# Optimization experiments

Hardware: AMD Instinct MI355X
Metric: run time of the kernel (lower is better)

Reference implementation:

```python
import jax, jax.numpy as jnp
import numpy as np

S, R, HC = 38, 340, 128      # num_s, num_r, h_channels
SC, RC, NO = 4, 3, 7          # s_channels, r_channels, num_o
L = 4                         # num_layers
B = 512                       # graphs per batch
N = B * (S + R)               # total nodes = 193536
E = 3_072_000                 # total edges
EPS = 1e-5


def leaky(x):
    return jnp.where(x > 0, x, 0.2 * x)


def batchnorm(x, w, b):
    # BatchNorm1d in training mode: batch stats, biased variance
    m = jnp.mean(x, axis=0)
    v = jnp.var(x, axis=0)
    return (x - m) * jax.lax.rsqrt(v + EPS) * w + b


def setup_inputs() -> dict:
    key = jax.random.key(0)
    ks = jax.random.split(key, 16)
    f32 = jnp.float32

    def w(k, shape, fan_in):
        return jax.random.normal(k, shape, f32) * (1.0 / np.sqrt(fan_in))

    return {
        "s_x": jax.random.normal(ks[0], (B * S, SC), f32),
        "r_x": jax.random.normal(ks[1], (B * R, RC + 5), f32),
        "edge_index": jax.random.randint(ks[2], (2, E), 0, N, dtype=jnp.int32),
        "bn_s_w": jnp.ones((SC,), f32),
        "bn_s_b": jnp.zeros((SC,), f32),
        "bn_r_w": jnp.ones((RC,), f32),
        "bn_r_b": jnp.zeros((RC,), f32),
        "lin_s_w": w(ks[3], (SC, HC), SC),
        "lin_r_w": w(ks[4], (RC, HC), RC),
        "conv_w": w(ks[5], (L, HC, HC), HC),
        "conv_b": jnp.zeros((L, HC), f32),
        "linr_w": w(ks[6], (S + R, NO), S + R),
        "linr_b": jnp.zeros((NO,), f32),
        "lino_w1": w(ks[7], (5, HC), 5),
        "lino_b1": jnp.zeros((HC,), f32),
        "lino_w2": w(ks[8], (HC, NO), HC),
        "lino_b2": jnp.zeros((NO,), f32),
    }


def reference(s_x, r_x, edge_index, bn_s_w, bn_s_b, bn_r_w, bn_r_b,
              lin_s_w, lin_r_w, conv_w, conv_b, linr_w, linr_b,
              lino_w1, lino_b1, lino_w2, lino_b2):
    Bn = r_x.shape[0] // R
    r_full = r_x.reshape(Bn, R, RC + 5)
    o_x = r_full[:, 0, RC:]                       # [B, 5]
    r = r_full[:, :, :RC].reshape(-1, RC)         # [B*R, 3]

    s = leaky(batchnorm(s_x, bn_s_w, bn_s_b) @ lin_s_w)   # [B*S, HC]
    r = leaky(batchnorm(r, bn_r_w, bn_r_b) @ lin_r_w)     # [B*R, HC]

    x = jnp.concatenate([s.reshape(Bn, S, HC), r.reshape(Bn, R, HC)], axis=1)
    x = x.reshape(-1, HC)                          # [N, HC]
    n = x.shape[0]

    # GCN normalization with self loops (computed once, shared by all layers)
    loops = jnp.arange(n, dtype=edge_index.dtype)
    src = jnp.concatenate([edge_index[0], loops])
    dst = jnp.concatenate([edge_index[1], loops])
    deg = jax.ops.segment_sum(jnp.ones_like(src, jnp.float32), dst, num_segments=n)
    dinv = jax.lax.rsqrt(deg)                      # deg >= 1 via self loops
    norm = (dinv[src] * dinv[dst])[:, None]        # [E+N, 1]

    for l in range(L):
        xw = x @ conv_w[l]                         # transform
        agg = jax.ops.segment_sum(norm * xw[src], dst, num_segments=n)
        x = x + leaky(agg + conv_b[l])             # residual + LeakyReLU

    pooled = x.reshape(Bn, S + R, HC).mean(axis=-1)  # adaptive_avg_pool1d over channels -> [B, 378]
    z = jnp.exp(pooled @ linr_w + linr_b)
    z = z / (jnp.sum(z, axis=1, keepdims=True) + 1.0)

    o = leaky(o_x @ lino_w1 + lino_b1) @ lino_w2 + lino_b2
    return z * jnp.exp(o)
```

## Files before the change

kernel.cpp:

```cpp
#include <hip/hip_runtime.h>
#include <hip/hip_bf16.h>

#define SDIM 38
#define RDIM 340
#define HC   128
#define SC   4
#define RC   3
#define NO   7
#define LCONV 4
#define BATCH 512
#define SR   378
#define NN   (BATCH*SR)
#define NS   (BATCH*SDIM)
#define NR   (BATCH*RDIM)
#define EE   3072000
#define EPSV 1e-5f
#define NBUK 756
#define BCAP 4800
#define BK_BLOCKS 256
#define BK_EDGES  12000
#define NSB 76

typedef short v8s __attribute__((ext_vector_type(8)));
typedef float v4f __attribute__((ext_vector_type(4)));
typedef float v2f __attribute__((ext_vector_type(2)));

__device__ __forceinline__ float leaky(float v){ return v > 0.f ? v : 0.2f*v; }

__device__ __forceinline__ unsigned short f2bf(float f){
    union { float f; unsigned u; } v; v.f = f;
    unsigned r = v.u + 0x7fffu + ((v.u >> 16) & 1u);
    return (unsigned short)(r >> 16);
}
__device__ __forceinline__ float4 bf4_to_f4(uint2 p){
    float4 r;
    r.x = __uint_as_float(p.x << 16);
    r.y = __uint_as_float(p.x & 0xffff0000u);
    r.z = __uint_as_float(p.y << 16);
    r.w = __uint_as_float(p.y & 0xffff0000u);
    return r;
}
__device__ __forceinline__ float4 fp8x4_to_f4(unsigned u){
    v2f lo = __builtin_amdgcn_cvt_pk_f32_fp8((int)u, false);
    v2f hi = __builtin_amdgcn_cvt_pk_f32_fp8((int)u, true);
    return make_float4(lo.x, lo.y, hi.x, hi.y);
}
__device__ __forceinline__ unsigned f4_to_fp8x4(float a, float b, float c, float d){
    int v = 0;
    v = __builtin_amdgcn_cvt_pk_fp8_f32(a, b, v, false);
    v = __builtin_amdgcn_cvt_pk_fp8_f32(c, d, v, true);
    return (unsigned)v;
}

__global__ void stats_kernel(const float* __restrict__ s_x, const float* __restrict__ r_x,
                             float* __restrict__ stats){
    int tid = threadIdx.x;
    __shared__ float sh[256][8];
    if (blockIdx.x < NSB){
        int r = blockIdx.x*256 + tid;
        float4 v = make_float4(0.f,0.f,0.f,0.f);
        if (r < NS) v = *(const float4*)(s_x + (size_t)r*SC);
        sh[tid][0]=v.x; sh[tid][1]=v.y; sh[tid][2]=v.z; sh[tid][3]=v.w;
        sh[tid][4]=v.x*v.x; sh[tid][5]=v.y*v.y; sh[tid][6]=v.z*v.z; sh[tid][7]=v.w*v.w;
        __syncthreads();
        for (int s=128; s>0; s>>=1){
            if (tid < s){
                #pragma unroll
                for (int k=0;k<8;k++) sh[tid][k]+=sh[tid+s][k];
            }
            __syncthreads();
        }
        if (tid < 8) atomicAdd(&stats[tid], sh[0][tid]);
    } else {
        int r = (blockIdx.x - NSB)*256 + tid;
        float4 v = make_float4(0.f,0.f,0.f,0.f);
        if (r < NR) v = *(const float4*)(r_x + (size_t)r*8);
        sh[tid][0]=v.x; sh[tid][1]=v.y; sh[tid][2]=v.z;
        sh[tid][3]=v.x*v.x; sh[tid][4]=v.y*v.y; sh[tid][5]=v.z*v.z;
        sh[tid][6]=0.f; sh[tid][7]=0.f;
        __syncthreads();
        for (int s=128; s>0; s>>=1){
            if (tid < s){
                #pragma unroll
                for (int k=0;k<6;k++) sh[tid][k]+=sh[tid+s][k];
            }
            __syncthreads();
        }
        if (tid < 6) atomicAdd(&stats[8+tid], sh[0][tid]);
    }
}

__global__ void finalize_stats_kernel(float* __restrict__ st,
        const float* __restrict__ bn_s_w, const float* __restrict__ bn_s_b,
        const float* __restrict__ bn_r_w, const float* __restrict__ bn_r_b){
    int t = threadIdx.x;
    if (t < SC){
        float m  = st[t] * (1.f/NS);
        float var= st[4+t] * (1.f/NS) - m*m;
        float sc = rsqrtf(var + EPSV) * bn_s_w[t];
        st[16+t] = sc; st[20+t] = bn_s_b[t] - m*sc;
    } else if (t >= 8 && t < 8+RC){
        int k = t-8;
        float m  = st[8+k] * (1.f/NR);
        float var= st[11+k] * (1.f/NR) - m*m;
        float sc = rsqrtf(var + EPSV) * bn_r_w[k];
        st[24+k] = sc; st[27+k] = bn_r_b[k] - m*sc;
    }
}

__global__ void feature_kernel(const float* __restrict__ s_x, const float* __restrict__ r_x,
        const float* __restrict__ stats, const float* __restrict__ lin_s_w,
        const float* __restrict__ lin_r_w, unsigned short* __restrict__ xb){
    int node = blockIdx.x*4 + (threadIdx.x >> 6);
    int c0 = (threadIdx.x & 63) * 2;
    int b = node / SR;
    int p = node - b*SR;
    float a0, a1;
    if (p < SDIM){
        int row = b*SDIM + p;
        float4 v = *(const float4*)(s_x + (size_t)row*SC);
        float i0 = v.x*stats[16]+stats[20];
        float i1 = v.y*stats[17]+stats[21];
        float i2 = v.z*stats[18]+stats[22];
        float i3 = v.w*stats[19]+stats[23];
        a0 = i0*lin_s_w[c0] + i1*lin_s_w[HC+c0] + i2*lin_s_w[2*HC+c0] + i3*lin_s_w[3*HC+c0];
        a1 = i0*lin_s_w[c0+1] + i1*lin_s_w[HC+c0+1] + i2*lin_s_w[2*HC+c0+1] + i3*lin_s_w[3*HC+c0+1];
    } else {
        int row = b*RDIM + (p - SDIM);
        float4 v = *(const float4*)(r_x + (size_t)row*8);
        float i0 = v.x*stats[24]+stats[27];
        float i1 = v.y*stats[25]+stats[28];
        float i2 = v.z*stats[26]+stats[29];
        a0 = i0*lin_r_w[c0] + i1*lin_r_w[HC+c0] + i2*lin_r_w[2*HC+c0];
        a1 = i0*lin_r_w[c0+1] + i1*lin_r_w[HC+c0+1] + i2*lin_r_w[2*HC+c0+1];
    }
    a0 = leaky(a0); a1 = leaky(a1);
    unsigned pk = (unsigned)f2bf(a0) | ((unsigned)f2bf(a1) << 16);
    *(unsigned*)(xb + (size_t)node*HC + c0) = pk;
}

__global__ __launch_bounds__(256) void bucket_kernel(const int* __restrict__ src,
        const int* __restrict__ dst, int* __restrict__ bcnt,
        unsigned* __restrict__ bedge){
    __shared__ int hist[NBUK];
    __shared__ int cur[NBUK];
    int tid = threadIdx.x;
    int e0 = blockIdx.x * BK_EDGES;
    for (int b = tid; b < NBUK; b += 256) hist[b] = 0;
    __syncthreads();
    for (int j = tid; j < BK_EDGES; j += 256){
        int d = dst[e0 + j];
        atomicAdd(&hist[d >> 8], 1);
    }
    __syncthreads();
    for (int b = tid; b < NBUK; b += 256){
        int c = hist[b];
        cur[b] = (c > 0) ? atomicAdd(&bcnt[b], c) : 0;
    }
    __syncthreads();
    for (int j = tid; j < BK_EDGES; j += 256){
        int d = dst[e0 + j];
        int s = src[e0 + j];
        int b = d >> 8;
        int pos = atomicAdd(&cur[b], 1);
        bedge[(size_t)b*BCAP + pos] = ((unsigned)s << 8) | (unsigned)(d & 255);
    }
}

__global__ __launch_bounds__(256) void hist_kernel(const int* __restrict__ bcnt,
        int* __restrict__ bbase, const unsigned* __restrict__ bedge,
        int* __restrict__ rp, float* __restrict__ dinv){
    __shared__ int h[256];
    __shared__ int sc[256];
    __shared__ int pre[256];
    int b = blockIdx.x, tid = threadIdx.x;
    int ps = 0;
    for (int i = tid; i < NBUK; i += 256)
        if (i < b) ps += bcnt[i];
    pre[tid] = ps;
    h[tid] = 0;
    __syncthreads();
    for (int s=128; s>0; s>>=1){
        if (tid < s) pre[tid] += pre[tid+s];
        __syncthreads();
    }
    int base = pre[0];
    int n = bcnt[b];
    const unsigned* be = bedge + (size_t)b*BCAP;
    for (int j = tid; j < n; j += 256)
        atomicAdd(&h[be[j] & 255u], 1);
    __syncthreads();
    int v = h[tid];
    sc[tid] = v;
    __syncthreads();
    for (int off=1; off<256; off<<=1){
        int t = (tid >= off) ? sc[tid-off] : 0;
        __syncthreads();
        sc[tid] += t;
        __syncthreads();
    }
    int node = b*256 + tid;
    rp[node] = base + sc[tid] - v;
    dinv[node] = rsqrtf((float)(v + 1));
    if (tid == 0) bbase[b] = base;
    if (b == NBUK-1 && tid == 0) rp[NN] = EE;
}

__global__ __launch_bounds__(256) void build_kernel(const int* __restrict__ bcnt,
        const int* __restrict__ bbase, const unsigned* __restrict__ bedge,
        const int* __restrict__ rp, const float* __restrict__ dinv,
        int2* __restrict__ csr){
    __shared__ int cur[256];
    __shared__ float dlocal[256];
    __shared__ int2 stage[BCAP];
    int b = blockIdx.x, tid = threadIdx.x;
    int base = bbase[b];
    cur[tid] = rp[b*256 + tid] - base;
    dlocal[tid] = dinv[b*256 + tid];
    __syncthreads();
    int n = bcnt[b];
    const unsigned* be = bedge + (size_t)b*BCAP;
    for (int j = tid; j < n; j += 256){
        unsigned e = be[j];
        int dl = (int)(e & 255u);
        int s  = (int)(e >> 8);
        float w = dinv[s] * dlocal[dl];
        int pos = atomicAdd(&cur[dl], 1);
        stage[pos] = make_int2((int)((e & ~255u) >> 1), __float_as_int(w));
    }
    __syncthreads();
    int2* seg = csr + base;
    for (int j = tid; j < n; j += 256)
        seg[j] = stage[j];
}

__global__ void wswz_kernel(const float* __restrict__ conv_w, uint4* __restrict__ wswz){
    int l = blockIdx.x;
    const float* Wg = conv_w + (size_t)l*HC*HC;
    int tid = threadIdx.x;
    #pragma unroll
    for (int i=0;i<8;i++){
        int slot = tid + i*256;
        int g = slot >> 6;
        int ln = slot & 63;
        int nt = g >> 2, ks = g & 3;
        int q = ln >> 4, n = nt*16 + (ln & 15);
        int k0 = ks*32 + q*8;
        unsigned short h[8];
        #pragma unroll
        for (int j=0;j<8;j++) h[j] = f2bf(Wg[(size_t)(k0+j)*HC + n]);
        uint4 o;
        o.x = (unsigned)h[0] | ((unsigned)h[1]<<16);
        o.y = (unsigned)h[2] | ((unsigned)h[3]<<16);
        o.z = (unsigned)h[4] | ((unsigned)h[5]<<16);
        o.w = (unsigned)h[6] | ((unsigned)h[7]<<16);
        wswz[(size_t)l*2048 + slot] = o;
    }
}

__global__ __launch_bounds__(256) void gemm_kernel(const unsigned short* __restrict__ xb,
        const uint4* __restrict__ wswz, unsigned char* __restrict__ xw){
    __shared__ uint4 Wlds[2048];
    __shared__ unsigned short outb[64*136];
    int tid = threadIdx.x;
    #pragma unroll
    for (int i=0;i<8;i++){
        int slot = tid + i*256;
        Wlds[slot] = wswz[slot];
    }
    int lane = tid & 63, w = tid >> 6;
    int q = lane >> 4, m = lane & 15;
    int rowbase = blockIdx.x*128;
    v4f acc[2][8];
    #pragma unroll
    for (int rg=0;rg<2;rg++)
        #pragma unroll
        for (int nt=0;nt<8;nt++) acc[rg][nt] = (v4f){0.f,0.f,0.f,0.f};
    __syncthreads();
    #pragma unroll
    for (int rg=0; rg<2; rg++){
        int row = rowbase + rg*64 + w*16 + m;
        const v8s* arow = (const v8s*)(xb + (size_t)row*HC + q*8);
        #pragma unroll
        for (int ks=0; ks<4; ks++){
            v8s a = arow[ks*4];
            #pragma unroll
            for (int nt=0;nt<8;nt++){
                v8s b = *(const v8s*)&Wlds[(nt*4+ks)*64 + lane];
                acc[rg][nt] = __builtin_amdgcn_mfma_f32_16x16x32_bf16(a, b, acc[rg][nt], 0, 0, 0);
            }
        }
    }
    #pragma unroll
    for (int rg=0; rg<2; rg++){
        #pragma unroll
        for (int nt=0;nt<8;nt++){
            #pragma unroll
            for (int i=0;i<4;i++){
                outb[(w*16 + q*4 + i)*136 + nt*16 + m] = f2bf(acc[rg][nt][i]);
            }
        }
        __syncthreads();
        size_t gbase = (size_t)(rowbase + rg*64) * HC;
        #pragma unroll
        for (int i=0;i<4;i++){
            int c = tid + i*256;
            int r = c >> 4, j = c & 15;
            uint4 v = *(const uint4*)&outb[r*136 + j*8];
            float4 lo = bf4_to_f4(make_uint2(v.x, v.y));
            float4 hi = bf4_to_f4(make_uint2(v.z, v.w));
            uint2 o;
            o.x = f4_to_fp8x4(lo.x, lo.y, lo.z, lo.w);
            o.y = f4_to_fp8x4(hi.x, hi.y, hi.z, hi.w);
            *(uint2*)&xw[gbase + (size_t)r*HC + j*8] = o;
        }
        __syncthreads();
    }
}

__global__ __launch_bounds__(256) void agg_kernel(const unsigned char* __restrict__ xw,
        const int* __restrict__ rp, const int2* __restrict__ csr,
        const float* __restrict__ dinv, const float* __restrict__ bias,
        unsigned short* __restrict__ xb, float* __restrict__ pooled){
    int lane = threadIdx.x & 63;
    int node = blockIdx.x*4 + (threadIdx.x >> 6);
    int g  = lane >> 4;
    unsigned c8 = (lane & 15) * 8;
    int beg = rp[node], end = rp[node+1];

    float4 aL0 = make_float4(0.f,0.f,0.f,0.f), aH0 = aL0;
    float4 aL1 = aL0, aH1 = aL0;

    int j = beg + g;
    while (j + 4 < end){
        int2 e0 = csr[j];
        int2 e1 = csr[j+4];
        uint2 p0 = *(const uint2*)(xw + ((unsigned)e0.x + c8));
        uint2 p1 = *(const uint2*)(xw + ((unsigned)e1.x + c8));
        float w0 = __int_as_float(e0.y);
        float w1 = __int_as_float(e1.y);
        float4 lo0 = fp8x4_to_f4(p0.x);
        float4 hi0 = fp8x4_to_f4(p0.y);
        float4 lo1 = fp8x4_to_f4(p1.x);
        float4 hi1 = fp8x4_to_f4(p1.y);
        aL0.x += w0*lo0.x; aL0.y += w0*lo0.y; aL0.z += w0*lo0.z; aL0.w += w0*lo0.w;
        aH0.x += w0*hi0.x; aH0.y += w0*hi0.y; aH0.z += w0*hi0.z; aH0.w += w0*hi0.w;
        aL1.x += w1*lo1.x; aL1.y += w1*lo1.y; aL1.z += w1*lo1.z; aL1.w += w1*lo1.w;
        aH1.x += w1*hi1.x; aH1.y += w1*hi1.y; aH1.z += w1*hi1.z; aH1.w += w1*hi1.w;
        j += 8;
    }
    while (j < end){
        int2 e = csr[j];
        uint2 p = *(const uint2*)(xw + ((unsigned)e.x + c8));
        float w = __int_as_float(e.y);
        float4 lo = fp8x4_to_f4(p.x);
        float4 hi = fp8x4_to_f4(p.y);
        aL0.x += w*lo.x; aL0.y += w*lo.y; aL0.z += w*lo.z; aL0.w += w*lo.w;
        aH0.x += w*hi.x; aH0.y += w*hi.y; aH0.z += w*hi.z; aH0.w += w*hi.w;
        j += 4;
    }
    aL0.x += aL1.x; aL0.y += aL1.y; aL0.z += aL1.z; aL0.w += aL1.w;
    aH0.x += aH1.x; aH0.y += aH1.y; aH0.z += aH1.z; aH0.w += aH1.w;
    if (g == 0){
        float dn = dinv[node];
        float sw = dn*dn;
        uint2 p = *(const uint2*)(xw + ((unsigned)node*HC + c8));
        float4 lo = fp8x4_to_f4(p.x);
        float4 hi = fp8x4_to_f4(p.y);
        aL0.x += sw*lo.x; aL0.y += sw*lo.y; aL0.z += sw*lo.z; aL0.w += sw*lo.w;
        aH0.x += sw*hi.x; aH0.y += sw*hi.y; aH0.z += sw*hi.z; aH0.w += sw*hi.w;
    }
    #pragma unroll
    for (int m2 = 16; m2 <= 32; m2 <<= 1){
        aL0.x += __shfl_xor(aL0.x, m2, 64);
        aL0.y += __shfl_xor(aL0.y, m2, 64);
        aL0.z += __shfl_xor(aL0.z, m2, 64);
        aL0.w += __shfl_xor(aL0.w, m2, 64);
        aH0.x += __shfl_xor(aH0.x, m2, 64);
        aH0.y += __shfl_xor(aH0.y, m2, 64);
        aH0.z += __shfl_xor(aH0.z, m2, 64);
        aH0.w += __shfl_xor(aH0.w, m2, 64);
    }
    if (g == 0){
        float4 bL = *(const float4*)(bias + c8);
        float4 bH = *(const float4*)(bias + c8 + 4);
        size_t idx = (size_t)node*HC + c8;
        uint4 xp = *(const uint4*)(xb + idx);
        float4 xL = bf4_to_f4(make_uint2(xp.x, xp.y));
        float4 xH = bf4_to_f4(make_uint2(xp.z, xp.w));
        xL.x += leaky(aL0.x + bL.x);
        xL.y += leaky(aL0.y + bL.y);
        xL.z += leaky(aL0.z + bL.z);
        xL.w += leaky(aL0.w + bL.w);
        xH.x += leaky(aH0.x + bH.x);
        xH.y += leaky(aH0.y + bH.y);
        xH.z += leaky(aH0.z + bH.z);
        xH.w += leaky(aH0.w + bH.w);
        if (pooled == nullptr){
            uint4 pk;
            pk.x = (unsigned)f2bf(xL.x) | ((unsigned)f2bf(xL.y) << 16);
            pk.y = (unsigned)f2bf(xL.z) | ((unsigned)f2bf(xL.w) << 16);
            pk.z = (unsigned)f2bf(xH.x) | ((unsigned)f2bf(xH.y) << 16);
            pk.w = (unsigned)f2bf(xH.z) | ((unsigned)f2bf(xH.w) << 16);
            *(uint4*)(xb + idx) = pk;
        } else {
            float s = xL.x + xL.y + xL.z + xL.w + xH.x + xH.y + xH.z + xH.w;
            #pragma unroll
            for (int m2 = 1; m2 < 16; m2 <<= 1)
                s += __shfl_xor(s, m2, 64);
            if (lane == 0) pooled[node] = s * (1.f/128.f);
        }
    }
}

__global__ void head_kernel(const float* __restrict__ pooled, const float* __restrict__ r_x,
        const float* __restrict__ linr_w, const float* __restrict__ linr_b,
        const float* __restrict__ lino_w1, const float* __restrict__ lino_b1,
        const float* __restrict__ lino_w2, const float* __restrict__ lino_b2,
        float* __restrict__ out){
    int b = blockIdx.x, tid = threadIdx.x;
    __shared__ float red[128][8];
    __shared__ float hsh[128];
    __shared__ float zsh[8];
    float part[NO];
    #pragma unroll
    for (int j=0;j<NO;j++) part[j]=0.f;
    for (int i = tid; i < SR; i += 128){
        float pv = pooled[(size_t)b*SR + i];
        #pragma unroll
        for (int j=0;j<NO;j++) part[j] += pv * linr_w[i*NO + j];
    }
    #pragma unroll
    for (int j=0;j<NO;j++) red[tid][j] = part[j];
    const float* ox = r_x + (size_t)b*RDIM*8 + RC;
    float hv = lino_b1[tid];
    #pragma unroll
    for (int k=0;k<5;k++) hv += ox[k]*lino_w1[k*HC + tid];
    hsh[tid] = leaky(hv);
    __syncthreads();
    for (int s=64; s>0; s>>=1){
        if (tid < s){
            #pragma unroll
            for (int j=0;j<NO;j++) red[tid][j] += red[tid+s][j];
        }
        __syncthreads();
    }
    if (tid < NO) zsh[tid] = expf(red[0][tid] + linr_b[tid]);
    __syncthreads();
    if (tid < NO){
        float zsum = 0.f;
        #pragma unroll
        for (int j=0;j<NO;j++) zsum += zsh[j];
        float z = zsh[tid] / (zsum + 1.f);
        float o = lino_b2[tid];
        for (int cc=0; cc<HC; cc++) o += hsh[cc]*lino_w2[cc*NO + tid];
        out[b*NO + tid] = z * expf(o);
    }
}

extern "C" void kernel_launch(void* const* d_in, const int* in_sizes, int n_in,
                              void* d_out, int out_size, void* d_ws, size_t ws_size,
                              hipStream_t stream) {
    const float* s_x     = (const float*)d_in[0];
    const float* r_x     = (const float*)d_in[1];
    const int*   ei      = (const int*)d_in[2];
    const float* bn_s_w  = (const float*)d_in[3];
    const float* bn_s_b  = (const float*)d_in[4];
    const float* bn_r_w  = (const float*)d_in[5];
    const float* bn_r_b  = (const float*)d_in[6];
    const float* lin_s_w = (const float*)d_in[7];
    const float* lin_r_w = (const float*)d_in[8];
    const float* conv_w  = (const float*)d_in[9];
    const float* conv_b  = (const float*)d_in[10];
    const float* linr_w  = (const float*)d_in[11];
    const float* linr_b  = (const float*)d_in[12];
    const float* lino_w1 = (const float*)d_in[13];
    const float* lino_b1 = (const float*)d_in[14];
    const float* lino_w2 = (const float*)d_in[15];
    const float* lino_b2 = (const float*)d_in[16];
    float* out = (float*)d_out;

    char* ws = (char*)d_ws;
    size_t off = 0;
    auto alloc = [&](size_t bytes)->void*{
        void* p = ws + off;
        off = (off + bytes + 255) & ~(size_t)255;
        return p;
    };
    unsigned short* xb = (unsigned short*)alloc((size_t)NN*HC*2);
    unsigned char*  xw = (unsigned char*) alloc((size_t)NN*HC);
    float* dinv     = (float*)alloc((size_t)NN*4);
    int*   rp       = (int*)  alloc((size_t)(NN+1)*4);
    int2*  csr      = (int2*) alloc((size_t)EE*8);
    unsigned* bedge = (unsigned*)alloc((size_t)NBUK*BCAP*4);
    int*   bcnt     = (int*)  alloc((size_t)NBUK*4);
    int*   bbase    = (int*)  alloc((size_t)NBUK*4);
    float* stats    = (float*)alloc(64*4);
    float* pooled   = (float*)alloc((size_t)NN*4);
    uint4* wswz     = (uint4*)alloc((size_t)LCONV*2048*16);

    hipMemsetAsync(bcnt, 0, (size_t)NBUK*4, stream);
    hipMemsetAsync(stats, 0, 64*4, stream);

    stats_kernel<<<NSB + (NR+255)/256, 256, 0, stream>>>(s_x, r_x, stats);
    finalize_stats_kernel<<<1, 64, 0, stream>>>(stats, bn_s_w, bn_s_b, bn_r_w, bn_r_b);
    feature_kernel<<<NN/4, 256, 0, stream>>>(s_x, r_x, stats, lin_s_w, lin_r_w, xb);
    wswz_kernel<<<LCONV, 256, 0, stream>>>(conv_w, wswz);

    bucket_kernel<<<BK_BLOCKS, 256, 0, stream>>>(ei, ei + EE, bcnt, bedge);
    hist_kernel<<<NBUK, 256, 0, stream>>>(bcnt, bbase, bedge, rp, dinv);
    build_kernel<<<NBUK, 256, 0, stream>>>(bcnt, bbase, bedge, rp, dinv, csr);

    for (int l = 0; l < LCONV; l++){
        gemm_kernel<<<NN/128, 256, 0, stream>>>(xb, wswz + (size_t)l*2048, xw);
        agg_kernel<<<NN/4, 256, 0, stream>>>(xw, rp, csr, dinv, conv_b + (size_t)l*HC,
                                             xb, (l == LCONV-1) ? pooled : nullptr);
    }

    head_kernel<<<BATCH, 128, 0, stream>>>(pooled, r_x, linr_w, linr_b,
                                           lino_w1, lino_b1, lino_w2, lino_b2, out);
}
```

Measured before the change: 744.6 us.

## Store node features in MFMA-panel layout and use packed fp8 conversion in aggregation

The bf16 node feature buffer moves from row-major to a 16-row panel layout that matches the MFMA A-operand fragment order. The GEMM can then read each lane's fragment as one contiguous coalesced 16-byte load per panel instead of strided row loads. The feature and aggregation kernels are changed to write and read this layout, and the feature kernel now produces 8 channels per thread. The aggregation accumulators are also rewritten as packed float2 multiply-adds on the pk fp8 conversions. The risk is that the residual read-modify-write in aggregation now does scattered 16-byte accesses into panels.

```diff
diff --git a/kernel.cpp b/kernel.cpp
--- a/kernel.cpp
+++ b/kernel.cpp
@@ -21,6 +21,7 @@
 #define BK_EDGES  12000
 #define NSB 76
 
+
 typedef short v8s __attribute__((ext_vector_type(8)));
 typedef float v4f __attribute__((ext_vector_type(4)));
 typedef float v2f __attribute__((ext_vector_type(2)));
@@ -39,11 +40,6 @@
     r.z = __uint_as_float(p.y << 16);
     r.w = __uint_as_float(p.y & 0xffff0000u);
     return r;
-}
-__device__ __forceinline__ float4 fp8x4_to_f4(unsigned u){
-    v2f lo = __builtin_amdgcn_cvt_pk_f32_fp8((int)u, false);
-    v2f hi = __builtin_amdgcn_cvt_pk_f32_fp8((int)u, true);
-    return make_float4(lo.x, lo.y, hi.x, hi.y);
 }
 __device__ __forceinline__ unsigned f4_to_fp8x4(float a, float b, float c, float d){
     int v = 0;
@@ -108,35 +104,47 @@
     }
 }
 
-__global__ void feature_kernel(const float* __restrict__ s_x, const float* __restrict__ r_x,
-        const float* __restrict__ stats, const float* __restrict__ lin_s_w,
-        const float* __restrict__ lin_r_w, unsigned short* __restrict__ xb){
-    int node = blockIdx.x*4 + (threadIdx.x >> 6);
-    int c0 = (threadIdx.x & 63) * 2;
+__global__ __launch_bounds__(256) void feature_kernel(const float* __restrict__ s_x,
+        const float* __restrict__ r_x, const float* __restrict__ stats,
+        const float* __restrict__ lin_s_w, const float* __restrict__ lin_r_w,
+        unsigned short* __restrict__ xb){
+    int p = blockIdx.x;
+    int tid = threadIdx.x;
+    int m = tid & 15;
+    int l = tid >> 4;
+    int c0 = l*8;
+    int node = p*16 + m;
     int b = node / SR;
-    int p = node - b*SR;
-    float a0, a1;
-    if (p < SDIM){
-        int row = b*SDIM + p;
+    int pp = node - b*SR;
+    float a[8];
+    if (pp < SDIM){
+        int row = b*SDIM + pp;
         float4 v = *(const float4*)(s_x + (size_t)row*SC);
         float i0 = v.x*stats[16]+stats[20];
         float i1 = v.y*stats[17]+stats[21];
         float i2 = v.z*stats[18]+stats[22];
         float i3 = v.w*stats[19]+stats[23];
-        a0 = i0*lin_s_w[c0] + i1*lin_s_w[HC+c0] + i2*lin_s_w[2*HC+c0] + i3*lin_s_w[3*HC+c0];
-        a1 = i0*lin_s_w[c0+1] + i1*lin_s_w[HC+c0+1] + i2*lin_s_w[2*HC+c0+1] + i3*lin_s_w[3*HC+c0+1];
+        #pragma unroll
+        for (int k=0;k<8;k++)
+            a[k] = i0*lin_s_w[c0+k] + i1*lin_s_w[HC+c0+k]
+                 + i2*lin_s_w[2*HC+c0+k] + i3*lin_s_w[3*HC+c0+k];
     } else {
-        int row = b*RDIM + (p - SDIM);
+        int row = b*RDIM + (pp - SDIM);
         float4 v = *(const float4*)(r_x + (size_t)row*8);
         float i0 = v.x*stats[24]+stats[27];
         float i1 = v.y*stats[25]+stats[28];
         float i2 = v.z*stats[26]+stats[29];
-        a0 = i0*lin_r_w[c0] + i1*lin_r_w[HC+c0] + i2*lin_r_w[2*HC+c0];
-        a1 = i0*lin_r_w[c0+1] + i1*lin_r_w[HC+c0+1] + i2*lin_r_w[2*HC+c0+1];
-    }
-    a0 = leaky(a0); a1 = leaky(a1);
-    unsigned pk = (unsigned)f2bf(a0) | ((unsigned)f2bf(a1) << 16);
-    *(unsigned*)(xb + (size_t)node*HC + c0) = pk;
+        #pragma unroll
+        for (int k=0;k<8;k++)
+            a[k] = i0*lin_r_w[c0+k] + i1*lin_r_w[HC+c0+k] + i2*lin_r_w[2*HC+c0+k];
+    }
+    uint4 pk;
+    pk.x = (unsigned)f2bf(leaky(a[0])) | ((unsigned)f2bf(leaky(a[1])) << 16);
+    pk.y = (unsigned)f2bf(leaky(a[2])) | ((unsigned)f2bf(leaky(a[3])) << 16);
+    pk.z = (unsigned)f2bf(leaky(a[4])) | ((unsigned)f2bf(leaky(a[5])) << 16);
+    pk.w = (unsigned)f2bf(leaky(a[6])) | ((unsigned)f2bf(leaky(a[7])) << 16);
+    size_t elem = (size_t)p*2048 + (size_t)((l>>2)*512 + (l&3)*128 + m*8);
+    *(uint4*)(xb + elem) = pk;
 }
 
 __global__ __launch_bounds__(256) void bucket_kernel(const int* __restrict__ src,
@@ -270,7 +278,6 @@
     }
     int lane = tid & 63, w = tid >> 6;
     int q = lane >> 4, m = lane & 15;
-    int rowbase = blockIdx.x*128;
     v4f acc[2][8];
     #pragma unroll
     for (int rg=0;rg<2;rg++)
@@ -279,11 +286,11 @@
     __syncthreads();
     #pragma unroll
     for (int rg=0; rg<2; rg++){
-        int row = rowbase + rg*64 + w*16 + m;
-        const v8s* arow = (const v8s*)(xb + (size_t)row*HC + q*8);
+        int p = blockIdx.x*8 + rg*4 + w;
+        const v8s* apan = (const v8s*)(xb + (size_t)p*2048);
         #pragma unroll
         for (int ks=0; ks<4; ks++){
-            v8s a = arow[ks*4];
+            v8s a = apan[ks*64 + lane];
             #pragma unroll
             for (int nt=0;nt<8;nt++){
                 v8s b = *(const v8s*)&Wlds[(nt*4+ks)*64 + lane];
@@ -291,6 +298,7 @@
             }
         }
     }
+    int rowbase = blockIdx.x*128;
     #pragma unroll
     for (int rg=0; rg<2; rg++){
         #pragma unroll
@@ -328,8 +336,8 @@
     unsigned c8 = (lane & 15) * 8;
     int beg = rp[node], end = rp[node+1];
 
-    float4 aL0 = make_float4(0.f,0.f,0.f,0.f), aH0 = aL0;
-    float4 aL1 = aL0, aH1 = aL0;
+    v2f a0[4] = {(v2f){0.f,0.f},(v2f){0.f,0.f},(v2f){0.f,0.f},(v2f){0.f,0.f}};
+    v2f a1[4] = {(v2f){0.f,0.f},(v2f){0.f,0.f},(v2f){0.f,0.f},(v2f){0.f,0.f}};
 
     int j = beg + g;
     while (j + 4 < end){
@@ -339,63 +347,64 @@
         uint2 p1 = *(const uint2*)(xw + ((unsigned)e1.x + c8));
         float w0 = __int_as_float(e0.y);
         float w1 = __int_as_float(e1.y);
-        float4 lo0 = fp8x4_to_f4(p0.x);
-        float4 hi0 = fp8x4_to_f4(p0.y);
-        float4 lo1 = fp8x4_to_f4(p1.x);
-        float4 hi1 = fp8x4_to_f4(p1.y);
-        aL0.x += w0*lo0.x; aL0.y += w0*lo0.y; aL0.z += w0*lo0.z; aL0.w += w0*lo0.w;
-        aH0.x += w0*hi0.x; aH0.y += w0*hi0.y; aH0.z += w0*hi0.z; aH0.w += w0*hi0.w;
-        aL1.x += w1*lo1.x; aL1.y += w1*lo1.y; aL1.z += w1*lo1.z; aL1.w += w1*lo1.w;
-        aH1.x += w1*hi1.x; aH1.y += w1*hi1.y; aH1.z += w1*hi1.z; aH1.w += w1*hi1.w;
+        v2f w0v = (v2f){w0, w0};
+        v2f w1v = (v2f){w1, w1};
+        a0[0] += w0v * __builtin_amdgcn_cvt_pk_f32_fp8((int)p0.x, false);
+        a0[1] += w0v * __builtin_amdgcn_cvt_pk_f32_fp8((int)p0.x, true);
+        a0[2] += w0v * __builtin_amdgcn_cvt_pk_f32_fp8((int)p0.y, false);
+        a0[3] += w0v * __builtin_amdgcn_cvt_pk_f32_fp8((int)p0.y, true);
+        a1[0] += w1v * __builtin_amdgcn_cvt_pk_f32_fp8((int)p1.x, false);
+        a1[1] += w1v * __builtin_amdgcn_cvt_pk_f32_fp8((int)p1.x, true);
+        a1[2] += w1v * __builtin_amdgcn_cvt_pk_f32_fp8((int)p1.y, false);
+        a1[3] += w1v * __builtin_amdgcn_cvt_pk_f32_fp8((int)p1.y, true);
         j += 8;
     }
     while (j < end){
         int2 e = csr[j];
         uint2 p = *(const uint2*)(xw + ((unsigned)e.x + c8));
         float w = __int_as_float(e.y);
-        float4 lo = fp8x4_to_f4(p.x);
-        float4 hi = fp8x4_to_f4(p.y);
-        aL0.x += w*lo.x; aL0.y += w*lo.y; aL0.z += w*lo.z; aL0.w += w*lo.w;
-        aH0.x += w*hi.x; aH0.y += w*hi.y; aH0.z += w*hi.z; aH0.w += w*hi.w;
+        v2f wv = (v2f){w, w};
+        a0[0] += wv * __builtin_amdgcn_cvt_pk_f32_fp8((int)p.x, false);
+        a0[1] += wv * __builtin_amdgcn_cvt_pk_f32_fp8((int)p.x, true);
+        a0[2] += wv * __builtin_amdgcn_cvt_pk_f32_fp8((int)p.y, false);
+        a0[3] += wv * __builtin_amdgcn_cvt_pk_f32_fp8((int)p.y, true);
         j += 4;
     }
-    aL0.x += aL1.x; aL0.y += aL1.y; aL0.z += aL1.z; aL0.w += aL1.w;
-    aH0.x += aH1.x; aH0.y += aH1.y; aH0.z += aH1.z; aH0.w += aH1.w;
+    #pragma unroll
+    for (int k=0;k<4;k++) a0[k] += a1[k];
     if (g == 0){
         float dn = dinv[node];
-        float sw = dn*dn;
+        v2f sw = (v2f){dn*dn, dn*dn};
         uint2 p = *(const uint2*)(xw + ((unsigned)node*HC + c8));
-        float4 lo = fp8x4_to_f4(p.x);
-        float4 hi = fp8x4_to_f4(p.y);
-        aL0.x += sw*lo.x; aL0.y += sw*lo.y; aL0.z += sw*lo.z; aL0.w += sw*lo.w;
-        aH0.x += sw*hi.x; aH0.y += sw*hi.y; aH0.z += sw*hi.z; aH0.w += sw*hi.w;
-    }
+        a0[0] += sw * __builtin_amdgcn_cvt_pk_f32_fp8((int)p.x, false);
+        a0[1] += sw * __builtin_amdgcn_cvt_pk_f32_fp8((int)p.x, true);
+        a0[2] += sw * __builtin_amdgcn_cvt_pk_f32_fp8((int)p.y, false);
+        a0[3] += sw * __builtin_amdgcn_cvt_pk_f32_fp8((int)p.y, true);
+    }
+    float r[8];
+    #pragma unroll
+    for (int k=0;k<4;k++){ r[2*k] = a0[k].x; r[2*k+1] = a0[k].y; }
     #pragma unroll
     for (int m2 = 16; m2 <= 32; m2 <<= 1){
-        aL0.x += __shfl_xor(aL0.x, m2, 64);
-        aL0.y += __shfl_xor(aL0.y, m2, 64);
-        aL0.z += __shfl_xor(aL0.z, m2, 64);
-        aL0.w += __shfl_xor(aL0.w, m2, 64);
-        aH0.x += __shfl_xor(aH0.x, m2, 64);
-        aH0.y += __shfl_xor(aH0.y, m2, 64);
-        aH0.z += __shfl_xor(aH0.z, m2, 64);
-        aH0.w += __shfl_xor(aH0.w, m2, 64);
+        #pragma unroll
+        for (int k=0;k<8;k++) r[k] += __shfl_xor(r[k], m2, 64);
     }
     if (g == 0){
         float4 bL = *(const float4*)(bias + c8);
         float4 bH = *(const float4*)(bias + c8 + 4);
-        size_t idx = (size_t)node*HC + c8;
+        size_t idx = (size_t)(node >> 4)*2048
+                   + (size_t)(((lane >> 2)*512) + ((lane & 3)*128) + ((node & 15)*8));
         uint4 xp = *(const uint4*)(xb + idx);
         float4 xL = bf4_to_f4(make_uint2(xp.x, xp.y));
         float4 xH = bf4_to_f4(make_uint2(xp.z, xp.w));
-        xL.x += leaky(aL0.x + bL.x);
-        xL.y += leaky(aL0.y + bL.y);
-        xL.z += leaky(aL0.z + bL.z);
-        xL.w += leaky(aL0.w + bL.w);
-        xH.x += leaky(aH0.x + bH.x);
-        xH.y += leaky(aH0.y + bH.y);
-        xH.z += leaky(aH0.z + bH.z);
-        xH.w += leaky(aH0.w + bH.w);
+        xL.x += leaky(r[0] + bL.x);
+        xL.y += leaky(r[1] + bL.y);
+        xL.z += leaky(r[2] + bL.z);
+        xL.w += leaky(r[3] + bL.w);
+        xH.x += leaky(r[4] + bH.x);
+        xH.y += leaky(r[5] + bH.y);
+        xH.z += leaky(r[6] + bH.z);
+        xH.w += leaky(r[7] + bH.w);
         if (pooled == nullptr){
             uint4 pk;
             pk.x = (unsigned)f2bf(xL.x) | ((unsigned)f2bf(xL.y) << 16);
@@ -504,7 +513,7 @@
 
     stats_kernel<<<NSB + (NR+255)/256, 256, 0, stream>>>(s_x, r_x, stats);
     finalize_stats_kernel<<<1, 64, 0, stream>>>(stats, bn_s_w, bn_s_b, bn_r_w, bn_r_b);
-    feature_kernel<<<NN/4, 256, 0, stream>>>(s_x, r_x, stats, lin_s_w, lin_r_w, xb);
+    feature_kernel<<<NN/16, 256, 0, stream>>>(s_x, r_x, stats, lin_s_w, lin_r_w, xb);
     wswz_kernel<<<LCONV, 256, 0, stream>>>(conv_w, wswz);
 
     bucket_kernel<<<BK_BLOCKS, 256, 0, stream>>>(ei, ei + EE, bcnt, bedge);
```

New measurement: 746.5 us. No clear change (+0.3%).

## Permute weight columns so MFMA output writes fp8 rows directly, drop LDS staging

Applied to the files above, without the earlier changes.

The weight swizzle now permutes output channels so that each lane's 8 accumulator tiles map to 8 consecutive columns. That lets the GEMM pack fp8 straight from registers and store to global memory, removing the LDS output buffer, its barriers and the bf16 round-trip. Each block also covers 256 rows instead of 128, which halves the grid and amortises the weight load into LDS. The trade-off is fewer blocks in flight, and the stores are now 8-byte writes scattered across rows.

```diff
diff --git a/kernel.cpp b/kernel.cpp
--- a/kernel.cpp
+++ b/kernel.cpp
@@ -244,11 +244,12 @@
         int g = slot >> 6;
         int ln = slot & 63;
         int nt = g >> 2, ks = g & 3;
-        int q = ln >> 4, n = nt*16 + (ln & 15);
+        int q = ln >> 4;
+        int ch = (ln & 15)*8 + nt;
         int k0 = ks*32 + q*8;
         unsigned short h[8];
         #pragma unroll
-        for (int j=0;j<8;j++) h[j] = f2bf(Wg[(size_t)(k0+j)*HC + n]);
+        for (int j=0;j<8;j++) h[j] = f2bf(Wg[(size_t)(k0+j)*HC + ch]);
         uint4 o;
         o.x = (unsigned)h[0] | ((unsigned)h[1]<<16);
         o.y = (unsigned)h[2] | ((unsigned)h[3]<<16);
@@ -261,7 +262,6 @@
 __global__ __launch_bounds__(256) void gemm_kernel(const unsigned short* __restrict__ xb,
         const uint4* __restrict__ wswz, unsigned char* __restrict__ xw){
     __shared__ uint4 Wlds[2048];
-    __shared__ unsigned short outb[64*136];
     int tid = threadIdx.x;
     #pragma unroll
     for (int i=0;i<8;i++){
@@ -270,51 +270,32 @@
     }
     int lane = tid & 63, w = tid >> 6;
     int q = lane >> 4, m = lane & 15;
-    int rowbase = blockIdx.x*128;
-    v4f acc[2][8];
-    #pragma unroll
-    for (int rg=0;rg<2;rg++)
-        #pragma unroll
-        for (int nt=0;nt<8;nt++) acc[rg][nt] = (v4f){0.f,0.f,0.f,0.f};
-    __syncthreads();
-    #pragma unroll
-    for (int rg=0; rg<2; rg++){
+    int rowbase = blockIdx.x*256;
+    __syncthreads();
+    #pragma unroll
+    for (int rg=0; rg<4; rg++){
         int row = rowbase + rg*64 + w*16 + m;
         const v8s* arow = (const v8s*)(xb + (size_t)row*HC + q*8);
+        v4f acc[8];
+        #pragma unroll
+        for (int nt=0;nt<8;nt++) acc[nt] = (v4f){0.f,0.f,0.f,0.f};
         #pragma unroll
         for (int ks=0; ks<4; ks++){
             v8s a = arow[ks*4];
             #pragma unroll
             for (int nt=0;nt<8;nt++){
                 v8s b = *(const v8s*)&Wlds[(nt*4+ks)*64 + lane];
-                acc[rg][nt] = __builtin_amdgcn_mfma_f32_16x16x32_bf16(a, b, acc[rg][nt], 0, 0, 0);
+                acc[nt] = __builtin_amdgcn_mfma_f32_16x16x32_bf16(a, b, acc[nt], 0, 0, 0);
             }
         }
-    }
-    #pragma unroll
-    for (int rg=0; rg<2; rg++){
-        #pragma unroll
-        for (int nt=0;nt<8;nt++){
-            #pragma unroll
-            for (int i=0;i<4;i++){
-                outb[(w*16 + q*4 + i)*136 + nt*16 + m] = f2bf(acc[rg][nt][i]);
-            }
-        }
-        __syncthreads();
-        size_t gbase = (size_t)(rowbase + rg*64) * HC;
+        size_t gbase = (size_t)(rowbase + rg*64 + w*16) * HC;
         #pragma unroll
         for (int i=0;i<4;i++){
-            int c = tid + i*256;
-            int r = c >> 4, j = c & 15;
-            uint4 v = *(const uint4*)&outb[r*136 + j*8];
-            float4 lo = bf4_to_f4(make_uint2(v.x, v.y));
-            float4 hi = bf4_to_f4(make_uint2(v.z, v.w));
             uint2 o;
-            o.x = f4_to_fp8x4(lo.x, lo.y, lo.z, lo.w);
-            o.y = f4_to_fp8x4(hi.x, hi.y, hi.z, hi.w);
-            *(uint2*)&xw[gbase + (size_t)r*HC + j*8] = o;
+            o.x = f4_to_fp8x4(acc[0][i], acc[1][i], acc[2][i], acc[3][i]);
+            o.y = f4_to_fp8x4(acc[4][i], acc[5][i], acc[6][i], acc[7][i]);
+            *(uint2*)&xw[gbase + (size_t)(q*4 + i)*HC + m*8] = o;
         }
-        __syncthreads();
     }
 }
 
@@ -512,7 +493,7 @@
     build_kernel<<<NBUK, 256, 0, stream>>>(bcnt, bbase, bedge, rp, dinv, csr);
 
     for (int l = 0; l < LCONV; l++){
-        gemm_kernel<<<NN/128, 256, 0, stream>>>(xb, wswz + (size_t)l*2048, xw);
+        gemm_kernel<<<NN/256, 256, 0, stream>>>(xb, wswz + (size_t)l*2048, xw);
         agg_kernel<<<NN/4, 256, 0, stream>>>(xw, rp, csr, dinv, conv_b + (size_t)l*HC,
                                              xb, (l == LCONV-1) ? pooled : nullptr);
     }
```

Measured after the change: 730.0 us, median of 2. 1.02x faster.
